# Optimization experiments

Hardware: AMD Instinct MI355X
Metric: run time of the kernel (lower is better)

Reference implementation:

```python
import jax, jax.numpy as jnp
import numpy as np

N, E = 50000, 800000
C_IN, C_HID, C_OUT = 64, 128, 64
BN_EPS = 1e-5


def setup_inputs() -> dict:
    key = jax.random.key(0)
    ks = jax.random.split(key, 8)
    s1 = 1.0 / np.sqrt(C_IN)
    s2 = 1.0 / np.sqrt(C_HID)
    return {
        "x": jax.random.normal(ks[0], (N, C_IN), dtype=jnp.float32),
        "edge_index": jax.random.randint(ks[1], (2, E), 0, N, dtype=jnp.int64),
        # message MLP: in -> hidden -> out
        "W1": jax.random.uniform(ks[2], (C_IN, C_HID), jnp.float32, -s1, s1),
        "b1": jnp.zeros((C_HID,), jnp.float32),
        "W2": jax.random.uniform(ks[3], (C_HID, C_OUT), jnp.float32, -s2, s2),
        "b2": jnp.zeros((C_OUT,), jnp.float32),
        # root/self transform
        "W_root": jax.random.uniform(ks[4], (C_IN, C_OUT), jnp.float32, -s1, s1),
        "b_root": jnp.zeros((C_OUT,), jnp.float32),
        # PReLU (single shared parameter, torch default 0.25)
        "prelu_w": jnp.full((1,), 0.25, jnp.float32),
        # BatchNorm affine params
        "bn_gamma": jnp.ones((C_OUT,), jnp.float32),
        "bn_beta": jnp.zeros((C_OUT,), jnp.float32),
    }


def reference(x, edge_index, W1, b1, W2, b2, W_root, b_root, prelu_w, bn_gamma, bn_beta):
    src, dst = edge_index[0], edge_index[1]
    # gather -> per-edge message MLP: [E, C_hid] -> [E, C_out]
    m = jax.nn.relu(x[src] @ W1 + b1) @ W2 + b2
    # scatter-sum to destination nodes: [N, C_out]
    agg = jax.ops.segment_sum(m, dst, num_segments=N)
    h = agg + x @ W_root + b_root
    # PReLU
    h = jnp.where(h >= 0, h, prelu_w * h)
    # BatchNorm over nodes (training-mode batch stats, biased var)
    mu = jnp.mean(h, axis=0)
    var = jnp.mean(jnp.square(h - mu), axis=0)
    h = (h - mu) * jax.lax.rsqrt(var + BN_EPS) * bn_gamma + bn_beta
    return h
```

## Files before the change

### kernel.cpp

```cpp
#include <hip/hip_runtime.h>

#define NNODES 50000
#define NEDGES 800000
#define NTILES 3125
#define CAP    64

typedef __attribute__((ext_vector_type(8))) short bf16x8;
typedef __attribute__((ext_vector_type(4))) float f32x4;

union FragU { uint u[4]; bf16x8 v; };

__device__ __forceinline__ uint bfr(float f) {
    uint u = __float_as_uint(f);
    return (u + 0x7fffu + ((u >> 16) & 1u)) >> 16;
}
__device__ __forceinline__ uint pack_bf2(float a, float b) {
    return bfr(a) | (bfr(b) << 16);
}
__device__ __forceinline__ float bf2f(uint hi16) {
    return __uint_as_float(hi16 << 16);
}

__global__ __launch_bounds__(256) void prep_kernel(
    const float* __restrict__ W1, const float* __restrict__ b1,
    const float* __restrict__ W2, const float* __restrict__ b2,
    const float* __restrict__ Wr, const float* __restrict__ br,
    uint* __restrict__ tbl, int* __restrict__ cnt, float* __restrict__ stats)
{
    const int f = blockIdx.x;
    const int tid = threadIdx.x;
    if (f < 40) {
        const int ln = tid >> 2, dd = tid & 3;
        const int g = ln >> 4, r = ln & 15;
        const int j0 = 2 * dd;
        float w0, w1v;
        if (f < 16) {
            const int mt = f >> 1, ks = f & 1;
            const int k = 32 * ks + 8 * g + j0, c = 16 * mt + r;
            w0 = W1[k * 128 + c];  w1v = W1[(k + 1) * 128 + c];
        } else if (f < 32) {
            const int mt = (f - 16) >> 2, ks = (f - 16) & 3;
            const int k = 32 * ks + 8 * g + j0, c = 16 * mt + r;
            w0 = W2[k * 64 + c];   w1v = W2[(k + 1) * 64 + c];
        } else {
            const int mt = (f - 32) >> 1, ks = (f - 32) & 1;
            const int k = 32 * ks + 8 * g + j0, c = 16 * mt + r;
            w0 = Wr[k * 64 + c];   w1v = Wr[(k + 1) * 64 + c];
        }
        tbl[f * 256 + tid] = pack_bf2(w0, w1v);
    } else if (f == 40) {
        if (tid < 128) tbl[10240 + tid] = __float_as_uint(b1[tid]);
        if (tid < 64) {
            tbl[10368 + tid] = __float_as_uint(b2[tid]);
            tbl[10432 + tid] = __float_as_uint(br[tid]);
        }
    } else {
        const int idx = (f - 41) * 256 + tid;
        if (idx < NNODES) cnt[idx] = 0;
        if (f == 41 && tid < 128) stats[tid] = 0.f;
    }
}

__global__ __launch_bounds__(256) void mlp_root_kernel(
    const float* __restrict__ x, const uint* __restrict__ tbl,
    ushort* __restrict__ M16, float* __restrict__ R)
{
    __shared__ uint sTab[10496];
    __shared__ uint sH[4 * 16 * 68];

    const int tid = threadIdx.x;
    {
        uint4* s4 = (uint4*)sTab;
        const uint4* t4 = (const uint4*)tbl;
        for (int i = tid; i < 2624; i += 256) s4[i] = t4[i];
    }
    __syncthreads();
    const uint*  sFrag = sTab;
    const float* sb1 = (const float*)&sTab[10240];
    const float* sb2 = (const float*)&sTab[10368];
    const float* sbr = (const float*)&sTab[10432];

    const int lane = tid & 63;
    const int g = lane >> 4, r = lane & 15;
    uint* Hw = &sH[(tid >> 6) * 16 * 68];
    uint* Mu = (uint*)M16;
    const int gw  = blockIdx.x * 4 + (tid >> 6);
    const int nwv = gridDim.x * 4;

#define LOADFRAG(f) (*(const bf16x8*)&sFrag[((f) << 8) | (lane << 2)])

    for (int t = gw; t < NTILES; t += nwv) {
        const int node = t * 16 + r;
        bf16x8 xf[2];
#pragma unroll
        for (int ks = 0; ks < 2; ++ks) {
            const float4 f0 = *(const float4*)&x[node * 64 + 32 * ks + 8 * g];
            const float4 f1 = *(const float4*)&x[node * 64 + 32 * ks + 8 * g + 4];
            FragU fx;
            fx.u[0] = pack_bf2(f0.x, f0.y); fx.u[1] = pack_bf2(f0.z, f0.w);
            fx.u[2] = pack_bf2(f1.x, f1.y); fx.u[3] = pack_bf2(f1.z, f1.w);
            xf[ks] = fx.v;
        }
#pragma unroll
        for (int mt = 0; mt < 8; ++mt) {
            f32x4 a = {0.f, 0.f, 0.f, 0.f};
            a = __builtin_amdgcn_mfma_f32_16x16x32_bf16(LOADFRAG(2 * mt), xf[0], a, 0, 0, 0);
            a = __builtin_amdgcn_mfma_f32_16x16x32_bf16(LOADFRAG(2 * mt + 1), xf[1], a, 0, 0, 0);
            const int hc = 16 * mt + 4 * g;
            const float v0 = fmaxf(a[0] + sb1[hc + 0], 0.f);
            const float v1 = fmaxf(a[1] + sb1[hc + 1], 0.f);
            const float v2 = fmaxf(a[2] + sb1[hc + 2], 0.f);
            const float v3 = fmaxf(a[3] + sb1[hc + 3], 0.f);
            const int hd = r * 68 + 8 * mt + 2 * g;
            Hw[hd]     = pack_bf2(v0, v1);
            Hw[hd + 1] = pack_bf2(v2, v3);
        }
        bf16x8 hf[4];
#pragma unroll
        for (int ks = 0; ks < 4; ++ks)
            hf[ks] = *(const bf16x8*)&Hw[r * 68 + 16 * ks + 4 * g];
#pragma unroll
        for (int mt = 0; mt < 4; ++mt) {
            f32x4 a2 = {0.f, 0.f, 0.f, 0.f};
#pragma unroll
            for (int ks = 0; ks < 4; ++ks)
                a2 = __builtin_amdgcn_mfma_f32_16x16x32_bf16(LOADFRAG(16 + 4 * mt + ks), hf[ks], a2, 0, 0, 0);
            f32x4 ar = {0.f, 0.f, 0.f, 0.f};
            ar = __builtin_amdgcn_mfma_f32_16x16x32_bf16(LOADFRAG(32 + 2 * mt), xf[0], ar, 0, 0, 0);
            ar = __builtin_amdgcn_mfma_f32_16x16x32_bf16(LOADFRAG(32 + 2 * mt + 1), xf[1], ar, 0, 0, 0);
            const int oc = 16 * mt + 4 * g;
            const float m0 = a2[0] + sb2[oc + 0], m1 = a2[1] + sb2[oc + 1];
            const float m2 = a2[2] + sb2[oc + 2], m3 = a2[3] + sb2[oc + 3];
            uint2 mp = make_uint2(pack_bf2(m0, m1), pack_bf2(m2, m3));
            *(uint2*)&Mu[node * 32 + 8 * mt + 2 * g] = mp;
            float4 rv = make_float4(ar[0] + sbr[oc + 0], ar[1] + sbr[oc + 1],
                                    ar[2] + sbr[oc + 2], ar[3] + sbr[oc + 3]);
            *(float4*)&R[node * 64 + oc] = rv;
        }
    }
#undef LOADFRAG
}

__global__ __launch_bounds__(256) void fill_kernel(
    const int* __restrict__ ei, int* __restrict__ cnt, ushort* __restrict__ bucketU)
{
    const int e = blockIdx.x * 256 + threadIdx.x;
    const int dst = ei[NEDGES + e];
    const int pos = atomicAdd(&cnt[dst], 1);
    if (pos < CAP) bucketU[dst * CAP + pos] = (ushort)ei[e];
}

__global__ __launch_bounds__(256) void gather_prelu_stats_kernel(
    const int* __restrict__ cnt, const ushort* __restrict__ bucketU,
    const uint2* __restrict__ M8, const float* __restrict__ pw,
    float* __restrict__ h, float* __restrict__ stats)
{
    __shared__ float ls[128];
    const int tid = threadIdx.x;
    if (tid < 128) ls[tid] = 0.f;
    __syncthreads();

    const int lane = tid & 63;
    const int q    = lane >> 4;
    const int u    = lane & 15;
    const int gw   = (blockIdx.x * 256 + tid) >> 6;
    const int nwv  = (gridDim.x * 256) >> 6;
    const float p  = pw[0];
    float sum = 0.f, sumsq = 0.f;

    int   cN  = 0, svN = 0;
    float hvN = 0.f;
    if (gw < NNODES) {
        cN  = cnt[gw];
        svN = (int)bucketU[gw * 64 + lane];
        hvN = h[gw * 64 + lane];
    }

    for (int n = gw; n < NNODES; n += nwv) {
        int c = cN; c = c > CAP ? CAP : c;
        const int   sv = svN;
        const float hv = hvN;

        uint2 mv[8];
#pragma unroll
        for (int j = 0; j < 8; ++j) {
            const int idx = 4 * j + q;
            const int s = __shfl(sv, (idx < c) ? idx : 0);
            mv[j] = M8[s * 16 + u];
        }

        const int nn = n + nwv;
        if (nn < NNODES) {
            cN  = cnt[nn];
            svN = (int)bucketU[nn * 64 + lane];
            hvN = h[nn * 64 + lane];
        }

        float a0 = 0.f, a1 = 0.f, a2 = 0.f, a3 = 0.f;
        float b0 = 0.f, b1 = 0.f, b2 = 0.f, b3 = 0.f;
#pragma unroll
        for (int j = 0; j < 8; ++j) {
            const bool ok = (4 * j + q) < c;
            const uint lo = ok ? mv[j].x : 0u;
            const uint hi = ok ? mv[j].y : 0u;
            if (j & 1) {
                b0 += bf2f(lo & 0xffffu); b1 += bf2f(lo >> 16);
                b2 += bf2f(hi & 0xffffu); b3 += bf2f(hi >> 16);
            } else {
                a0 += bf2f(lo & 0xffffu); a1 += bf2f(lo >> 16);
                a2 += bf2f(hi & 0xffffu); a3 += bf2f(hi >> 16);
            }
        }
        if (c > 32) {
            for (int i = 32; i < c; i += 4) {
                const int idx = i + q;
                const int s = __shfl(sv, (idx < c) ? idx : 0);
                const uint2 m = M8[s * 16 + u];
                const bool ok = idx < c;
                const uint lo = ok ? m.x : 0u;
                const uint hi = ok ? m.y : 0u;
                a0 += bf2f(lo & 0xffffu); a1 += bf2f(lo >> 16);
                a2 += bf2f(hi & 0xffffu); a3 += bf2f(hi >> 16);
            }
        }
        a0 += b0; a1 += b1; a2 += b2; a3 += b3;

        a0 += __shfl_xor(a0, 16); a0 += __shfl_xor(a0, 32);
        a1 += __shfl_xor(a1, 16); a1 += __shfl_xor(a1, 32);
        a2 += __shfl_xor(a2, 16); a2 += __shfl_xor(a2, 32);
        a3 += __shfl_xor(a3, 16); a3 += __shfl_xor(a3, 32);

        const int srcl = lane >> 2;
        const float t0 = __shfl(a0, srcl), t1 = __shfl(a1, srcl);
        const float t2 = __shfl(a2, srcl), t3 = __shfl(a3, srcl);
        const float e01 = (lane & 1) ? t1 : t0;
        const float e23 = (lane & 1) ? t3 : t2;
        float v = hv + ((lane & 2) ? e23 : e01);
        v = (v >= 0.f) ? v : p * v;
        h[n * 64 + lane] = v;
        sum += v;
        sumsq = fmaf(v, v, sumsq);
    }
    atomicAdd(&ls[lane], sum);
    atomicAdd(&ls[64 + lane], sumsq);
    __syncthreads();
    if (tid < 128) atomicAdd(&stats[tid], ls[tid]);
}

__global__ __launch_bounds__(256) void bn_kernel(
    float4* __restrict__ h, const float* __restrict__ stats,
    const float* __restrict__ gamma, const float* __restrict__ beta)
{
    const int i  = blockIdx.x * 256 + threadIdx.x;
    const int c0 = (i & 15) * 4;
    const float inv = 1.0f / (float)NNODES;
    const float4 s1 = *(const float4*)&stats[c0];
    const float4 s2 = *(const float4*)&stats[64 + c0];
    const float4 gm = *(const float4*)&gamma[c0];
    const float4 bt = *(const float4*)&beta[c0];
    float4 v = h[i];
    float mu, var;
    mu = s1.x * inv; var = s2.x * inv - mu * mu; v.x = (v.x - mu) * (gm.x * rsqrtf(var + 1e-5f)) + bt.x;
    mu = s1.y * inv; var = s2.y * inv - mu * mu; v.y = (v.y - mu) * (gm.y * rsqrtf(var + 1e-5f)) + bt.y;
    mu = s1.z * inv; var = s2.z * inv - mu * mu; v.z = (v.z - mu) * (gm.z * rsqrtf(var + 1e-5f)) + bt.z;
    mu = s1.w * inv; var = s2.w * inv - mu * mu; v.w = (v.w - mu) * (gm.w * rsqrtf(var + 1e-5f)) + bt.w;
    h[i] = v;
}

extern "C" void kernel_launch(void* const* d_in, const int* in_sizes, int n_in,
                              void* d_out, int out_size, void* d_ws, size_t ws_size,
                              hipStream_t stream) {
    const float* x     = (const float*)d_in[0];
    const int*   ei    = (const int*)d_in[1];
    const float* W1    = (const float*)d_in[2];
    const float* b1    = (const float*)d_in[3];
    const float* W2    = (const float*)d_in[4];
    const float* b2    = (const float*)d_in[5];
    const float* Wr    = (const float*)d_in[6];
    const float* br    = (const float*)d_in[7];
    const float* pw    = (const float*)d_in[8];
    const float* gamma = (const float*)d_in[9];
    const float* beta  = (const float*)d_in[10];

    float* out = (float*)d_out;

    char* ws = (char*)d_ws;
    ushort* M16    = (ushort*)ws;
    ushort* bucketU= (ushort*)(ws + 6400000);
    int*    cnt    = (int*)(ws + 12800000);
    float*  stats  = (float*)(ws + 12800000 + 200000);
    uint*   tbl    = (uint*)(ws + 12800000 + 200000 + 512);

    prep_kernel<<<237, 256, 0, stream>>>(W1, b1, W2, b2, Wr, br, tbl, cnt, stats);
    fill_kernel<<<NEDGES / 256, 256, 0, stream>>>(ei, cnt, bucketU);
    mlp_root_kernel<<<512, 256, 0, stream>>>(x, tbl, M16, out);
    gather_prelu_stats_kernel<<<2048, 256, 0, stream>>>(cnt, bucketU, (const uint2*)M16, pw, out, stats);
    bn_kernel<<<3125, 256, 0, stream>>>((float4*)out, stats, gamma, beta);
}
```

Before: 214.1 us.

## Keep MLP weight fragments in registers and process two nodes per gather iteration

The MLP kernel no longer copies the whole weight table into shared memory. It preloads 32 bf16 fragments for W1 and W2 into registers, reads the root-weight fragments straight from global memory, and launches half as many blocks. The gather kernel now handles two nodes per wave iteration with interleaved burst loads and prefetching two ahead, and it skips the second half of the initial burst when a node has 16 or fewer edges. These changes aim to raise memory-level parallelism and cut LDS traffic, at the cost of much higher register pressure, which can lower occupancy or cause spills.

```diff
diff --git a/kernel.cpp b/kernel.cpp
--- a/kernel.cpp
+++ b/kernel.cpp
@@ -65,29 +65,32 @@
     const float* __restrict__ x, const uint* __restrict__ tbl,
     ushort* __restrict__ M16, float* __restrict__ R)
 {
-    __shared__ uint sTab[10496];
-    __shared__ uint sH[4 * 16 * 68];
+    __shared__ uint  sH[4 * 16 * 68];
+    __shared__ float sb[256];
 
     const int tid = threadIdx.x;
-    {
-        uint4* s4 = (uint4*)sTab;
-        const uint4* t4 = (const uint4*)tbl;
-        for (int i = tid; i < 2624; i += 256) s4[i] = t4[i];
+    if (tid < 128) {
+        sb[tid]       = __uint_as_float(tbl[10240 + tid]);
+        sb[128 + tid] = __uint_as_float(tbl[10368 + tid]);
     }
     __syncthreads();
-    const uint*  sFrag = sTab;
-    const float* sb1 = (const float*)&sTab[10240];
-    const float* sb2 = (const float*)&sTab[10368];
-    const float* sbr = (const float*)&sTab[10432];
+    const float* sb1 = sb;
+    const float* sb2 = sb + 128;
+    const float* sbr = sb + 192;
 
     const int lane = tid & 63;
     const int g = lane >> 4, r = lane & 15;
     uint* Hw = &sH[(tid >> 6) * 16 * 68];
     uint* Mu = (uint*)M16;
+
+#define LDTBL(f) (*(const bf16x8*)&tbl[((f) << 8) | (lane << 2)])
+
+    bf16x8 wf[32];
+#pragma unroll
+    for (int f = 0; f < 32; ++f) wf[f] = LDTBL(f);
+
     const int gw  = blockIdx.x * 4 + (tid >> 6);
     const int nwv = gridDim.x * 4;
-
-#define LOADFRAG(f) (*(const bf16x8*)&sFrag[((f) << 8) | (lane << 2)])
 
     for (int t = gw; t < NTILES; t += nwv) {
         const int node = t * 16 + r;
@@ -104,8 +107,8 @@
 #pragma unroll
         for (int mt = 0; mt < 8; ++mt) {
             f32x4 a = {0.f, 0.f, 0.f, 0.f};
-            a = __builtin_amdgcn_mfma_f32_16x16x32_bf16(LOADFRAG(2 * mt), xf[0], a, 0, 0, 0);
-            a = __builtin_amdgcn_mfma_f32_16x16x32_bf16(LOADFRAG(2 * mt + 1), xf[1], a, 0, 0, 0);
+            a = __builtin_amdgcn_mfma_f32_16x16x32_bf16(wf[2 * mt], xf[0], a, 0, 0, 0);
+            a = __builtin_amdgcn_mfma_f32_16x16x32_bf16(wf[2 * mt + 1], xf[1], a, 0, 0, 0);
             const int hc = 16 * mt + 4 * g;
             const float v0 = fmaxf(a[0] + sb1[hc + 0], 0.f);
             const float v1 = fmaxf(a[1] + sb1[hc + 1], 0.f);
@@ -124,10 +127,10 @@
             f32x4 a2 = {0.f, 0.f, 0.f, 0.f};
 #pragma unroll
             for (int ks = 0; ks < 4; ++ks)
-                a2 = __builtin_amdgcn_mfma_f32_16x16x32_bf16(LOADFRAG(16 + 4 * mt + ks), hf[ks], a2, 0, 0, 0);
+                a2 = __builtin_amdgcn_mfma_f32_16x16x32_bf16(wf[16 + 4 * mt + ks], hf[ks], a2, 0, 0, 0);
             f32x4 ar = {0.f, 0.f, 0.f, 0.f};
-            ar = __builtin_amdgcn_mfma_f32_16x16x32_bf16(LOADFRAG(32 + 2 * mt), xf[0], ar, 0, 0, 0);
-            ar = __builtin_amdgcn_mfma_f32_16x16x32_bf16(LOADFRAG(32 + 2 * mt + 1), xf[1], ar, 0, 0, 0);
+            ar = __builtin_amdgcn_mfma_f32_16x16x32_bf16(LDTBL(32 + 2 * mt), xf[0], ar, 0, 0, 0);
+            ar = __builtin_amdgcn_mfma_f32_16x16x32_bf16(LDTBL(32 + 2 * mt + 1), xf[1], ar, 0, 0, 0);
             const int oc = 16 * mt + 4 * g;
             const float m0 = a2[0] + sb2[oc + 0], m1 = a2[1] + sb2[oc + 1];
             const float m2 = a2[2] + sb2[oc + 2], m3 = a2[3] + sb2[oc + 3];
@@ -138,7 +141,7 @@
             *(float4*)&R[node * 64 + oc] = rv;
         }
     }
-#undef LOADFRAG
+#undef LDTBL
 }
 
 __global__ __launch_bounds__(256) void fill_kernel(
@@ -150,66 +153,51 @@
     if (pos < CAP) bucketU[dst * CAP + pos] = (ushort)ei[e];
 }
 
-__global__ __launch_bounds__(256) void gather_prelu_stats_kernel(
-    const int* __restrict__ cnt, const ushort* __restrict__ bucketU,
-    const uint2* __restrict__ M8, const float* __restrict__ pw,
-    float* __restrict__ h, float* __restrict__ stats)
-{
-    __shared__ float ls[128];
-    const int tid = threadIdx.x;
-    if (tid < 128) ls[tid] = 0.f;
-    __syncthreads();
-
-    const int lane = tid & 63;
-    const int q    = lane >> 4;
-    const int u    = lane & 15;
-    const int gw   = (blockIdx.x * 256 + tid) >> 6;
-    const int nwv  = (gridDim.x * 256) >> 6;
-    const float p  = pw[0];
-    float sum = 0.f, sumsq = 0.f;
-
-    int   cN  = 0, svN = 0;
-    float hvN = 0.f;
-    if (gw < NNODES) {
-        cN  = cnt[gw];
-        svN = (int)bucketU[gw * 64 + lane];
-        hvN = h[gw * 64 + lane];
-    }
-
-    for (int n = gw; n < NNODES; n += nwv) {
-        int c = cN; c = c > CAP ? CAP : c;
-        const int   sv = svN;
-        const float hv = hvN;
-
-        uint2 mv[8];
-#pragma unroll
-        for (int j = 0; j < 8; ++j) {
+__device__ __forceinline__ void burst_load(const uint2* __restrict__ M8, int sv,
+                                           int c, int q, int u, uint2 mv[8])
+{
+#pragma unroll
+    for (int j = 0; j < 4; ++j) {
+        const int idx = 4 * j + q;
+        const int s = __shfl(sv, (idx < c) ? idx : 0);
+        mv[j] = M8[s * 16 + u];
+    }
+    if (c > 16) {
+#pragma unroll
+        for (int j = 4; j < 8; ++j) {
             const int idx = 4 * j + q;
             const int s = __shfl(sv, (idx < c) ? idx : 0);
             mv[j] = M8[s * 16 + u];
         }
-
-        const int nn = n + nwv;
-        if (nn < NNODES) {
-            cN  = cnt[nn];
-            svN = (int)bucketU[nn * 64 + lane];
-            hvN = h[nn * 64 + lane];
-        }
-
-        float a0 = 0.f, a1 = 0.f, a2 = 0.f, a3 = 0.f;
-        float b0 = 0.f, b1 = 0.f, b2 = 0.f, b3 = 0.f;
-#pragma unroll
-        for (int j = 0; j < 8; ++j) {
+    }
+}
+
+__device__ __forceinline__ void unpack_acc(const uint2 mv[8], int c, int q, int u,
+                                           const uint2* __restrict__ M8, int sv,
+                                           float& A0, float& A1, float& A2, float& A3)
+{
+    float a0 = 0.f, a1 = 0.f, a2 = 0.f, a3 = 0.f;
+    float b0 = 0.f, b1 = 0.f, b2 = 0.f, b3 = 0.f;
+#pragma unroll
+    for (int j = 0; j < 4; ++j) {
+        const bool ok = (4 * j + q) < c;
+        const uint lo = ok ? mv[j].x : 0u;
+        const uint hi = ok ? mv[j].y : 0u;
+        if (j & 1) { b0 += bf2f(lo & 0xffffu); b1 += bf2f(lo >> 16);
+                     b2 += bf2f(hi & 0xffffu); b3 += bf2f(hi >> 16); }
+        else       { a0 += bf2f(lo & 0xffffu); a1 += bf2f(lo >> 16);
+                     a2 += bf2f(hi & 0xffffu); a3 += bf2f(hi >> 16); }
+    }
+    if (c > 16) {
+#pragma unroll
+        for (int j = 4; j < 8; ++j) {
             const bool ok = (4 * j + q) < c;
             const uint lo = ok ? mv[j].x : 0u;
             const uint hi = ok ? mv[j].y : 0u;
-            if (j & 1) {
-                b0 += bf2f(lo & 0xffffu); b1 += bf2f(lo >> 16);
-                b2 += bf2f(hi & 0xffffu); b3 += bf2f(hi >> 16);
-            } else {
-                a0 += bf2f(lo & 0xffffu); a1 += bf2f(lo >> 16);
-                a2 += bf2f(hi & 0xffffu); a3 += bf2f(hi >> 16);
-            }
+            if (j & 1) { b0 += bf2f(lo & 0xffffu); b1 += bf2f(lo >> 16);
+                         b2 += bf2f(hi & 0xffffu); b3 += bf2f(hi >> 16); }
+            else       { a0 += bf2f(lo & 0xffffu); a1 += bf2f(lo >> 16);
+                         a2 += bf2f(hi & 0xffffu); a3 += bf2f(hi >> 16); }
         }
         if (c > 32) {
             for (int i = 32; i < c; i += 4) {
@@ -223,23 +211,83 @@
                 a2 += bf2f(hi & 0xffffu); a3 += bf2f(hi >> 16);
             }
         }
-        a0 += b0; a1 += b1; a2 += b2; a3 += b3;
-
-        a0 += __shfl_xor(a0, 16); a0 += __shfl_xor(a0, 32);
-        a1 += __shfl_xor(a1, 16); a1 += __shfl_xor(a1, 32);
-        a2 += __shfl_xor(a2, 16); a2 += __shfl_xor(a2, 32);
-        a3 += __shfl_xor(a3, 16); a3 += __shfl_xor(a3, 32);
-
-        const int srcl = lane >> 2;
-        const float t0 = __shfl(a0, srcl), t1 = __shfl(a1, srcl);
-        const float t2 = __shfl(a2, srcl), t3 = __shfl(a3, srcl);
-        const float e01 = (lane & 1) ? t1 : t0;
-        const float e23 = (lane & 1) ? t3 : t2;
-        float v = hv + ((lane & 2) ? e23 : e01);
-        v = (v >= 0.f) ? v : p * v;
-        h[n * 64 + lane] = v;
-        sum += v;
-        sumsq = fmaf(v, v, sumsq);
+    }
+    A0 = a0 + b0; A1 = a1 + b1; A2 = a2 + b2; A3 = a3 + b3;
+}
+
+__device__ __forceinline__ void combine_store(float a0, float a1, float a2, float a3,
+                                              float hv, float p, int lane,
+                                              float* __restrict__ hrow,
+                                              float& sum, float& sumsq)
+{
+    a0 += __shfl_xor(a0, 16); a0 += __shfl_xor(a0, 32);
+    a1 += __shfl_xor(a1, 16); a1 += __shfl_xor(a1, 32);
+    a2 += __shfl_xor(a2, 16); a2 += __shfl_xor(a2, 32);
+    a3 += __shfl_xor(a3, 16); a3 += __shfl_xor(a3, 32);
+    const int srcl = lane >> 2;
+    const float t0 = __shfl(a0, srcl), t1 = __shfl(a1, srcl);
+    const float t2 = __shfl(a2, srcl), t3 = __shfl(a3, srcl);
+    const float e01 = (lane & 1) ? t1 : t0;
+    const float e23 = (lane & 1) ? t3 : t2;
+    float v = hv + ((lane & 2) ? e23 : e01);
+    v = (v >= 0.f) ? v : p * v;
+    hrow[lane] = v;
+    sum += v;
+    sumsq = fmaf(v, v, sumsq);
+}
+
+__global__ __launch_bounds__(256) void gather_prelu_stats_kernel(
+    const int* __restrict__ cnt, const ushort* __restrict__ bucketU,
+    const uint2* __restrict__ M8, const float* __restrict__ pw,
+    float* __restrict__ h, float* __restrict__ stats)
+{
+    __shared__ float ls[128];
+    const int tid = threadIdx.x;
+    if (tid < 128) ls[tid] = 0.f;
+    __syncthreads();
+
+    const int lane = tid & 63;
+    const int q    = lane >> 4;
+    const int u    = lane & 15;
+    const int gw   = (blockIdx.x * 256 + tid) >> 6;
+    const int nwv  = (gridDim.x * 256) >> 6;
+    const float p  = pw[0];
+    float sum = 0.f, sumsq = 0.f;
+
+    int nA = gw, nB = gw + nwv;
+    int cA = 0, svA = 0; float hA = 0.f;
+    if (nA < NNODES) { cA = cnt[nA]; svA = (int)bucketU[nA * 64 + lane]; hA = h[nA * 64 + lane]; }
+    int cB = 0, svB = 0; float hB = 0.f;
+    if (nB < NNODES) { cB = cnt[nB]; svB = (int)bucketU[nB * 64 + lane]; hB = h[nB * 64 + lane]; }
+
+    while (nA < NNODES) {
+        const int  ca   = cA > CAP ? CAP : cA;
+        const int  cb   = cB > CAP ? CAP : cB;
+        const bool hasB = nB < NNODES;
+
+        uint2 mvA[8], mvB[8];
+        burst_load(M8, svA, ca, q, u, mvA);
+        if (hasB) burst_load(M8, svB, cb, q, u, mvB);
+
+        const int n2 = nA + 2 * nwv, n3 = nB + 2 * nwv;
+        int c2 = 0, s2 = 0; float h2 = 0.f;
+        int c3 = 0, s3 = 0; float h3 = 0.f;
+        if (n2 < NNODES) { c2 = cnt[n2]; s2 = (int)bucketU[n2 * 64 + lane]; h2 = h[n2 * 64 + lane]; }
+        if (n3 < NNODES) { c3 = cnt[n3]; s3 = (int)bucketU[n3 * 64 + lane]; h3 = h[n3 * 64 + lane]; }
+
+        float A0, A1, A2, A3;
+        unpack_acc(mvA, ca, q, u, M8, svA, A0, A1, A2, A3);
+        combine_store(A0, A1, A2, A3, hA, p, lane, &h[nA * 64], sum, sumsq);
+
+        if (hasB) {
+            float B0, B1, B2, B3;
+            unpack_acc(mvB, cb, q, u, M8, svB, B0, B1, B2, B3);
+            combine_store(B0, B1, B2, B3, hB, p, lane, &h[nB * 64], sum, sumsq);
+        }
+
+        nA = n2; nB = n3;
+        cA = c2; svA = s2; hA = h2;
+        cB = c3; svB = s3; hB = h3;
     }
     atomicAdd(&ls[lane], sum);
     atomicAdd(&ls[64 + lane], sumsq);
@@ -293,7 +341,7 @@
 
     prep_kernel<<<237, 256, 0, stream>>>(W1, b1, W2, b2, Wr, br, tbl, cnt, stats);
     fill_kernel<<<NEDGES / 256, 256, 0, stream>>>(ei, cnt, bucketU);
-    mlp_root_kernel<<<512, 256, 0, stream>>>(x, tbl, M16, out);
+    mlp_root_kernel<<<256, 256, 0, stream>>>(x, tbl, M16, out);
     gather_prelu_stats_kernel<<<2048, 256, 0, stream>>>(cnt, bucketU, (const uint2*)M16, pw, out, stats);
     bn_kernel<<<3125, 256, 0, stream>>>((float4*)out, stats, gamma, beta);
 }
```

Result: faster. 203.1 us (-5.1%).
